# Kernel tuning notes

Measured on AMD Instinct MI355X. Metric: run time of the kernel, lower is better.

The kernel has to match this reference:

```python
import jax, jax.numpy as jnp
import numpy as np


def setup_inputs() -> dict:
    key = jax.random.key(0)
    k1, k2 = jax.random.split(key)
    B, C, H, W = 8, 64, 128, 512
    image_tensor = jax.random.normal(k1, (B, C, H, W), dtype=jnp.float32)
    # positive metric depths in ~[1, 56] m
    depth = jax.random.uniform(k2, (B, H, W), dtype=jnp.float32) * 55.0 + 1.0
    fx = fy = 500.0; cx = 512.0; cy = 128.0  # intrinsics for original 1024x256 image
    camera_k = jnp.tile(jnp.array([[fx, 0.0, cx], [0.0, fy, cy], [0.0, 0.0, 1.0]],
                                  dtype=jnp.float32)[None], (B, 1, 1))
    meter_per_pixel = jnp.full((1,), 0.25, dtype=jnp.float32)
    return {"image_tensor": image_tensor, "camera_k": camera_k, "depth": depth,
            "meter_per_pixel": meter_per_pixel, "sat_width": 512,
            "ori_grdH": 256, "ori_grdW": 1024}


def reference(image_tensor, camera_k, depth, meter_per_pixel, sat_width, ori_grdH, ori_grdW):
    B, C, H, W = image_tensor.shape
    half = sat_width // 2
    mpp = meter_per_pixel.reshape(())

    # scale intrinsics from original image size to feature-map size (rows 0 and 1)
    row_scale = jnp.array([W / ori_grdW, H / ori_grdH, 1.0], dtype=jnp.float32)
    ck = camera_k * row_scale[None, :, None]
    k_inv = jnp.linalg.inv(ck)  # [B,3,3]

    # back-project pixel grid: xyz_w[b,h,w,:] = K^-1 @ [u,v,1]
    v, u = jnp.meshgrid(jnp.arange(H, dtype=jnp.float32),
                        jnp.arange(W, dtype=jnp.float32), indexing='ij')
    uv1 = jnp.stack([u, v, jnp.ones_like(u)], axis=-1)          # [H,W,3]
    xyz_w = jnp.einsum('bij,hwj->bhwi', k_inv, uv1)             # [B,H,W,3]
    # depth is already at (H,W): bilinear same-size resize is identity
    xyz = (xyz_w * depth[..., None] * 1.2).reshape(B * H * W, 3)

    feats = image_tensor.transpose(0, 2, 3, 1).reshape(B * H * W, C)

    # voxelize x,z (torch .long() truncates toward zero)
    x = jnp.trunc(xyz[:, 0] / mpp).astype(jnp.int32)
    z = jnp.trunc(xyz[:, 2] / mpp).astype(jnp.int32)
    y = xyz[:, 1]
    b = jnp.repeat(jnp.arange(B, dtype=jnp.int32), H * W)

    kept = (x >= -half) & (x <= half - 1) & (z >= -half) & (z <= half - 1)
    max_h = jnp.max(jnp.where(kept, y, -jnp.inf))
    xx = x + half
    zz = z + half
    h = max_h - y  # height key; the last entry per voxel (max h) survives dedup

    # voxel rank (same encoding as torch); out-of-bounds points get a sentinel
    rank0 = zz * (sat_width * B) + (xx + 1) * B + b
    SENT = sat_width * sat_width * B + B
    rank0 = jnp.where(kept, rank0, SENT)

    # torch: sort by h, then stable sort by rank0  == lexsort(primary=rank0, secondary=h)
    order = jnp.lexsort((h, rank0))
    r_s = rank0[order]
    f_s = feats[order]
    b_s, xx_s, zz_s = b[order], xx[order], zz[order]

    # keep the last point of each rank0 group (highest h in that voxel)
    is_last = jnp.concatenate([r_s[:-1] != r_s[1:], jnp.array([True])])
    valid = is_last & (r_s != SENT)

    flat = b_s * (sat_width * sat_width) + xx_s * sat_width + zz_s
    flat = jnp.where(valid, flat, B * sat_width * sat_width)  # invalid -> OOB, dropped

    final = jnp.zeros((B * sat_width * sat_width, C), dtype=jnp.float32)
    final = final.at[flat].set(f_s, mode='drop')
    return final.reshape(B, sat_width, sat_width, C).transpose(0, 3, 1, 2)
```

## Files before the change

### kernel.cpp

```cpp
#include <hip/hip_runtime.h>

#define BB 8
#define CC 64
#define HH 128
#define WW 512
#define SS 512
#define HALF 256
#define HWP (HH * WW)
#define BHW (BB * HWP)
#define CELLS (BB * SS * SS)

__device__ __forceinline__ unsigned int order_f32(float f) {
    unsigned int u = __float_as_uint(f);
    return (u & 0x80000000u) ? ~u : (u | 0x80000000u);
}

__global__ __launch_bounds__(256) void proj_kernel(
    const float* __restrict__ camera_k,
    const float* __restrict__ depth,
    const float* __restrict__ mpp_p,
    unsigned long long* __restrict__ keys)
{
    __shared__ float sk[9];
    const int idx = blockIdx.x * 256 + threadIdx.x;
    const int b = idx >> 16;

    if (threadIdx.x == 0) {
        const float rs[3] = {0.5f, 0.5f, 1.0f};
        double a[9];
        #pragma unroll
        for (int i = 0; i < 3; ++i)
            #pragma unroll
            for (int j = 0; j < 3; ++j)
                a[i*3 + j] = (double)__fmul_rn(camera_k[b*9 + i*3 + j], rs[i]);
        double det = a[0]*(a[4]*a[8]-a[5]*a[7])
                   - a[1]*(a[3]*a[8]-a[5]*a[6])
                   + a[2]*(a[3]*a[7]-a[4]*a[6]);
        double inv[9];
        inv[0] =  (a[4]*a[8]-a[5]*a[7])/det;
        inv[1] = -(a[1]*a[8]-a[2]*a[7])/det;
        inv[2] =  (a[1]*a[5]-a[2]*a[4])/det;
        inv[3] = -(a[3]*a[8]-a[5]*a[6])/det;
        inv[4] =  (a[0]*a[8]-a[2]*a[6])/det;
        inv[5] = -(a[0]*a[5]-a[2]*a[3])/det;
        inv[6] =  (a[3]*a[7]-a[4]*a[6])/det;
        inv[7] = -(a[0]*a[7]-a[1]*a[6])/det;
        inv[8] =  (a[0]*a[4]-a[1]*a[3])/det;
        #pragma unroll
        for (int i = 0; i < 9; ++i) sk[i] = (float)inv[i];
    }
    __syncthreads();

    const int rem = idx & (HWP - 1);
    const int v = rem >> 9;
    const int u = rem & (WW - 1);
    const float d = depth[idx];
    const float mpp = mpp_p[0];
    const float uf = (float)u, vf = (float)v;

    float xw = __fadd_rn(__fadd_rn(__fmul_rn(sk[0], uf), __fmul_rn(sk[1], vf)), sk[2]);
    float yw = __fadd_rn(__fadd_rn(__fmul_rn(sk[3], uf), __fmul_rn(sk[4], vf)), sk[5]);
    float zw = __fadd_rn(__fadd_rn(__fmul_rn(sk[6], uf), __fmul_rn(sk[7], vf)), sk[8]);
    float x3 = __fmul_rn(__fmul_rn(xw, d), 1.2f);
    float y3 = __fmul_rn(__fmul_rn(yw, d), 1.2f);
    float z3 = __fmul_rn(__fmul_rn(zw, d), 1.2f);

    int xi = (int)truncf(__fdiv_rn(x3, mpp));
    int zi = (int)truncf(__fdiv_rn(z3, mpp));

    if (xi >= -HALF && xi <= HALF - 1 && zi >= -HALF && zi <= HALF - 1) {
        int cell = (b << 18) | ((xi + HALF) << 9) | (zi + HALF);
        unsigned long long key =
            ((unsigned long long)order_f32(y3) << 32) | (unsigned int)(~idx);
        atomicMin(&keys[cell], key);
    }
}

__global__ __launch_bounds__(256) void transpose_kernel(
    const float* __restrict__ img,
    float* __restrict__ img_t)
{
    __shared__ float tile[64][65];
    const int gp0  = blockIdx.x * 64;
    const int b    = gp0 >> 16;
    const int p0   = gp0 & (HWP - 1);
    const int lane = threadIdx.x & 63;
    const int grp  = threadIdx.x >> 6;

    const float* src = img + (size_t)b * CC * HWP + p0;
    #pragma unroll
    for (int i = 0; i < 16; ++i) {
        int ch = grp * 16 + i;
        tile[lane][ch] = src[(size_t)ch * HWP + lane];
    }
    __syncthreads();
    float* dst = img_t + (size_t)gp0 * CC;
    #pragma unroll
    for (int i = 0; i < 16; ++i) {
        int p = grp * 16 + i;
        dst[(size_t)p * CC + lane] = tile[p][lane];
    }
}

__global__ __launch_bounds__(256) void scatter_kernel(
    const float* __restrict__ img_t,
    const unsigned long long* __restrict__ keys,
    float* __restrict__ out)
{
    __shared__ float sT[128 * 64];
    __shared__ int   sRem[128];

    const int cell0 = blockIdx.x * 128;
    const int b     = cell0 >> 18;
    const int t     = threadIdx.x;
    const int w     = t >> 6;
    const int l     = t & 63;

    if (t < 128) {
        unsigned long long k = keys[cell0 + t];
        sRem[t] = (k == ~0ull) ? -1
                : (int)((~(unsigned int)(k & 0xFFFFFFFFull)) & (HWP - 1));
    }
    __syncthreads();

    const size_t bHWP = (size_t)b * HWP;
    #pragma unroll 8
    for (int i = 0; i < 32; ++i) {
        int cell = w * 32 + i;
        int r = sRem[cell];
        float val = 0.0f;
        if (r >= 0)
            val = img_t[((bHWP + (size_t)r) << 6) + l];
        sT[(cell << 6) + (l ^ (cell & 31))] = val;
    }
    __syncthreads();

    const int local = cell0 & (SS * SS - 1);
    float* op = out + (size_t)b * CC * (SS * SS) + local;
    #pragma unroll
    for (int j = 0; j < 16; ++j) {
        int c = w * 16 + j;
        float v0 = sT[((l)      << 6) + (c ^ (l & 31))];
        float v1 = sT[((l + 64) << 6) + (c ^ (l & 31))];
        float* oc = op + (size_t)c * (SS * SS);
        oc[l]      = v0;
        oc[64 + l] = v1;
    }
}

extern "C" void kernel_launch(void* const* d_in, const int* in_sizes, int n_in,
                              void* d_out, int out_size, void* d_ws, size_t ws_size,
                              hipStream_t stream) {
    const float* img      = (const float*)d_in[0];
    const float* camera_k = (const float*)d_in[1];
    const float* depth    = (const float*)d_in[2];
    const float* mpp      = (const float*)d_in[3];

    unsigned long long* keys = (unsigned long long*)d_ws;
    float* img_t = (float*)((char*)d_ws + ((size_t)32 << 20));

    hipMemsetAsync(keys, 0xFF, (size_t)CELLS * sizeof(unsigned long long), stream);

    transpose_kernel<<<BHW / 64, 256, 0, stream>>>(img, img_t);
    proj_kernel<<<BHW / 256, 256, 0, stream>>>(camera_k, depth, mpp, keys);
    scatter_kernel<<<CELLS / 128, 256, 0, stream>>>(img_t, keys, (float*)d_out);
}
```

Baseline: 844.9 us.

## Shard atomic-min keys per XCC and fuse transpose into projection kernel

The projection kernel now reads the hardware XCC id and issues its atomic min into a per-XCC copy of the key array, using workgroup scope. This aims to keep the atomics in each die's local L2 and avoid cross-die coherence traffic. The scatter kernel then reduces the eight shards when it loads keys. The transpose is merged into the projection kernel, which saves one launch. In exchange the memset grows eightfold (128 MB) and the scatter kernel makes eight key reads per cell. Workgroup-scope atomics on global memory also depend on every block on the same XCC sharing an L2.

```diff
diff --git a/kernel.cpp b/kernel.cpp
--- a/kernel.cpp
+++ b/kernel.cpp
@@ -9,6 +9,7 @@
 #define HWP (HH * WW)
 #define BHW (BB * HWP)
 #define CELLS (BB * SS * SS)
+#define NSHARD 8
 
 __device__ __forceinline__ unsigned int order_f32(float f) {
     unsigned int u = __float_as_uint(f);
@@ -16,16 +17,22 @@
 }
 
 __global__ __launch_bounds__(256) void proj_kernel(
+    const float* __restrict__ img,
     const float* __restrict__ camera_k,
     const float* __restrict__ depth,
     const float* __restrict__ mpp_p,
-    unsigned long long* __restrict__ keys)
+    unsigned long long* __restrict__ keys8,
+    float* __restrict__ img_t)
 {
     __shared__ float sk[9];
-    const int idx = blockIdx.x * 256 + threadIdx.x;
-    const int b = idx >> 16;
+    __shared__ float tile[64][65];
 
-    if (threadIdx.x == 0) {
+    const int gp0 = blockIdx.x * 256;
+    const int b   = gp0 >> 16;
+    const int t   = threadIdx.x;
+    const int idx = gp0 + t;
+
+    if (t == 0) {
         const float rs[3] = {0.5f, 0.5f, 1.0f};
         double a[9];
         #pragma unroll
@@ -51,60 +58,64 @@
     }
     __syncthreads();
 
-    const int rem = idx & (HWP - 1);
-    const int v = rem >> 9;
-    const int u = rem & (WW - 1);
-    const float d = depth[idx];
-    const float mpp = mpp_p[0];
-    const float uf = (float)u, vf = (float)v;
+    {
+        const int rem = idx & (HWP - 1);
+        const int v = rem >> 9;
+        const int u = rem & (WW - 1);
+        const float d = depth[idx];
+        const float mpp = mpp_p[0];
+        const float uf = (float)u, vf = (float)v;
 
-    float xw = __fadd_rn(__fadd_rn(__fmul_rn(sk[0], uf), __fmul_rn(sk[1], vf)), sk[2]);
-    float yw = __fadd_rn(__fadd_rn(__fmul_rn(sk[3], uf), __fmul_rn(sk[4], vf)), sk[5]);
-    float zw = __fadd_rn(__fadd_rn(__fmul_rn(sk[6], uf), __fmul_rn(sk[7], vf)), sk[8]);
-    float x3 = __fmul_rn(__fmul_rn(xw, d), 1.2f);
-    float y3 = __fmul_rn(__fmul_rn(yw, d), 1.2f);
-    float z3 = __fmul_rn(__fmul_rn(zw, d), 1.2f);
+        float xw = __fadd_rn(__fadd_rn(__fmul_rn(sk[0], uf), __fmul_rn(sk[1], vf)), sk[2]);
+        float yw = __fadd_rn(__fadd_rn(__fmul_rn(sk[3], uf), __fmul_rn(sk[4], vf)), sk[5]);
+        float zw = __fadd_rn(__fadd_rn(__fmul_rn(sk[6], uf), __fmul_rn(sk[7], vf)), sk[8]);
+        float x3 = __fmul_rn(__fmul_rn(xw, d), 1.2f);
+        float y3 = __fmul_rn(__fmul_rn(yw, d), 1.2f);
+        float z3 = __fmul_rn(__fmul_rn(zw, d), 1.2f);
 
-    int xi = (int)truncf(__fdiv_rn(x3, mpp));
-    int zi = (int)truncf(__fdiv_rn(z3, mpp));
+        int xi = (int)truncf(__fdiv_rn(x3, mpp));
+        int zi = (int)truncf(__fdiv_rn(z3, mpp));
 
-    if (xi >= -HALF && xi <= HALF - 1 && zi >= -HALF && zi <= HALF - 1) {
-        int cell = (b << 18) | ((xi + HALF) << 9) | (zi + HALF);
-        unsigned long long key =
-            ((unsigned long long)order_f32(y3) << 32) | (unsigned int)(~idx);
-        atomicMin(&keys[cell], key);
+        if (xi >= -HALF && xi <= HALF - 1 && zi >= -HALF && zi <= HALF - 1) {
+            int cell = (b << 18) | ((xi + HALF) << 9) | (zi + HALF);
+            unsigned long long key =
+                ((unsigned long long)order_f32(y3) << 32) | (unsigned int)(~idx);
+            unsigned int xcc;
+            asm volatile("s_getreg_b32 %0, hwreg(HW_REG_XCC_ID)" : "=s"(xcc));
+            unsigned long long* shard = keys8 + (size_t)(xcc & (NSHARD - 1)) * CELLS;
+            __hip_atomic_fetch_min(&shard[cell], key,
+                                   __ATOMIC_RELAXED, __HIP_MEMORY_SCOPE_WORKGROUP);
+        }
     }
-}
 
-__global__ __launch_bounds__(256) void transpose_kernel(
-    const float* __restrict__ img,
-    float* __restrict__ img_t)
-{
-    __shared__ float tile[64][65];
-    const int gp0  = blockIdx.x * 64;
-    const int b    = gp0 >> 16;
+    const int lane = t & 63;
+    const int grp  = t >> 6;
     const int p0   = gp0 & (HWP - 1);
-    const int lane = threadIdx.x & 63;
-    const int grp  = threadIdx.x >> 6;
+    const float* src = img + (size_t)b * CC * HWP + p0;
+    float*       dst = img_t + (size_t)gp0 * CC;
 
-    const float* src = img + (size_t)b * CC * HWP + p0;
     #pragma unroll
-    for (int i = 0; i < 16; ++i) {
-        int ch = grp * 16 + i;
-        tile[lane][ch] = src[(size_t)ch * HWP + lane];
-    }
-    __syncthreads();
-    float* dst = img_t + (size_t)gp0 * CC;
-    #pragma unroll
-    for (int i = 0; i < 16; ++i) {
-        int p = grp * 16 + i;
-        dst[(size_t)p * CC + lane] = tile[p][lane];
+    for (int s4 = 0; s4 < 4; ++s4) {
+        __syncthreads();
+        const float* ssrc = src + s4 * 64;
+        #pragma unroll
+        for (int i = 0; i < 16; ++i) {
+            int ch = grp * 16 + i;
+            tile[lane][ch] = ssrc[(size_t)ch * HWP + lane];
+        }
+        __syncthreads();
+        float* sdst = dst + (size_t)(s4 * 64) * CC;
+        #pragma unroll
+        for (int i = 0; i < 16; ++i) {
+            int p = grp * 16 + i;
+            sdst[(size_t)p * CC + lane] = tile[p][lane];
+        }
     }
 }
 
 __global__ __launch_bounds__(256) void scatter_kernel(
     const float* __restrict__ img_t,
-    const unsigned long long* __restrict__ keys,
+    const unsigned long long* __restrict__ keys8,
     float* __restrict__ out)
 {
     __shared__ float sT[128 * 64];
@@ -117,7 +128,13 @@
     const int l     = t & 63;
 
     if (t < 128) {
-        unsigned long long k = keys[cell0 + t];
+        const unsigned long long* kp = keys8 + cell0 + t;
+        unsigned long long k = ~0ull;
+        #pragma unroll
+        for (int s = 0; s < NSHARD; ++s) {
+            unsigned long long ks = kp[(size_t)s * CELLS];
+            k = ks < k ? ks : k;
+        }
         sRem[t] = (k == ~0ull) ? -1
                 : (int)((~(unsigned int)(k & 0xFFFFFFFFull)) & (HWP - 1));
     }
@@ -156,12 +173,11 @@
     const float* depth    = (const float*)d_in[2];
     const float* mpp      = (const float*)d_in[3];
 
-    unsigned long long* keys = (unsigned long long*)d_ws;
-    float* img_t = (float*)((char*)d_ws + ((size_t)32 << 20));
+    unsigned long long* keys8 = (unsigned long long*)d_ws;
+    float* img_t = (float*)((char*)d_ws + ((size_t)128 << 20));
 
-    hipMemsetAsync(keys, 0xFF, (size_t)CELLS * sizeof(unsigned long long), stream);
+    hipMemsetAsync(keys8, 0xFF, (size_t)NSHARD * CELLS * sizeof(unsigned long long), stream);
 
-    transpose_kernel<<<BHW / 64, 256, 0, stream>>>(img, img_t);
-    proj_kernel<<<BHW / 256, 256, 0, stream>>>(camera_k, depth, mpp, keys);
-    scatter_kernel<<<CELLS / 128, 256, 0, stream>>>(img_t, keys, (float*)d_out);
+    proj_kernel<<<BHW / 256, 256, 0, stream>>>(img, camera_k, depth, mpp, keys8, img_t);
+    scatter_kernel<<<CELLS / 128, 256, 0, stream>>>(img_t, keys8, (float*)d_out);
 }
```

Result: no change. 854.5 us (+1.1%).

## Drop image transpose kernel and gather directly from channel-major planes

Applied to the files above, without the earlier changes.

Removes the full NCHW→NHWC transpose pass and has the scatter kernel gather each channel value straight from the original image planes. Per-cell source indices are preloaded into registers so 32 independent loads can be in flight per thread, and output writes become nontemporal stores. This saves a full read and write of the 128 MB image, but the gathers become strided and uncoalesced across channels. Each lane now reads from its own channel plane at scattered pixel positions.

```diff
diff --git a/kernel.cpp b/kernel.cpp
--- a/kernel.cpp
+++ b/kernel.cpp
@@ -76,34 +76,8 @@
     }
 }
 
-__global__ __launch_bounds__(256) void transpose_kernel(
+__global__ __launch_bounds__(256) void scatter_kernel(
     const float* __restrict__ img,
-    float* __restrict__ img_t)
-{
-    __shared__ float tile[64][65];
-    const int gp0  = blockIdx.x * 64;
-    const int b    = gp0 >> 16;
-    const int p0   = gp0 & (HWP - 1);
-    const int lane = threadIdx.x & 63;
-    const int grp  = threadIdx.x >> 6;
-
-    const float* src = img + (size_t)b * CC * HWP + p0;
-    #pragma unroll
-    for (int i = 0; i < 16; ++i) {
-        int ch = grp * 16 + i;
-        tile[lane][ch] = src[(size_t)ch * HWP + lane];
-    }
-    __syncthreads();
-    float* dst = img_t + (size_t)gp0 * CC;
-    #pragma unroll
-    for (int i = 0; i < 16; ++i) {
-        int p = grp * 16 + i;
-        dst[(size_t)p * CC + lane] = tile[p][lane];
-    }
-}
-
-__global__ __launch_bounds__(256) void scatter_kernel(
-    const float* __restrict__ img_t,
     const unsigned long long* __restrict__ keys,
     float* __restrict__ out)
 {
@@ -115,6 +89,7 @@
     const int t     = threadIdx.x;
     const int w     = t >> 6;
     const int l     = t & 63;
+    const int ci0   = w * 32;
 
     if (t < 128) {
         unsigned long long k = keys[cell0 + t];
@@ -123,15 +98,21 @@
     }
     __syncthreads();
 
-    const size_t bHWP = (size_t)b * HWP;
-    #pragma unroll 8
+    const float* plane = img + ((size_t)b * CC + (size_t)l) * HWP;
+
+    int rr[32];
+    #pragma unroll
+    for (int i = 0; i < 32; ++i) rr[i] = sRem[ci0 + i];
+
+    float vv[32];
+    #pragma unroll
+    for (int i = 0; i < 32; ++i)
+        vv[i] = (rr[i] >= 0) ? plane[rr[i]] : 0.0f;
+
+    #pragma unroll
     for (int i = 0; i < 32; ++i) {
-        int cell = w * 32 + i;
-        int r = sRem[cell];
-        float val = 0.0f;
-        if (r >= 0)
-            val = img_t[((bHWP + (size_t)r) << 6) + l];
-        sT[(cell << 6) + (l ^ (cell & 31))] = val;
+        int cell = ci0 + i;
+        sT[(cell << 6) + (l ^ (cell & 31))] = vv[i];
     }
     __syncthreads();
 
@@ -143,8 +124,8 @@
         float v0 = sT[((l)      << 6) + (c ^ (l & 31))];
         float v1 = sT[((l + 64) << 6) + (c ^ (l & 31))];
         float* oc = op + (size_t)c * (SS * SS);
-        oc[l]      = v0;
-        oc[64 + l] = v1;
+        __builtin_nontemporal_store(v0, &oc[l]);
+        __builtin_nontemporal_store(v1, &oc[64 + l]);
     }
 }
 
@@ -157,11 +138,9 @@
     const float* mpp      = (const float*)d_in[3];
 
     unsigned long long* keys = (unsigned long long*)d_ws;
-    float* img_t = (float*)((char*)d_ws + ((size_t)32 << 20));
 
     hipMemsetAsync(keys, 0xFF, (size_t)CELLS * sizeof(unsigned long long), stream);
 
-    transpose_kernel<<<BHW / 64, 256, 0, stream>>>(img, img_t);
     proj_kernel<<<BHW / 256, 256, 0, stream>>>(camera_k, depth, mpp, keys);
-    scatter_kernel<<<CELLS / 128, 256, 0, stream>>>(img_t, keys, (float*)d_out);
+    scatter_kernel<<<CELLS / 128, 256, 0, stream>>>(img, keys, (float*)d_out);
 }
```

Measured after the change: 837.3 us. No clear change (-0.9%).
